# Kernel tuning notes

Hardware: AMD Instinct MI355X
Metric: run time of the kernel (lower is better)

## Reference

```python
import jax, jax.numpy as jnp
import numpy as np

B, T, D = 2, 2048, 2048
H, HD = 8, 128
C = H * HD  # 1024 channels
BT = 64     # chunk size
EPS_RMS = 1.1920929e-07  # torch fp32 finfo eps (RMSNorm default)


def causal_dw_conv(x, w, b):
    # x: [B,T,C], w: [C,4], b: [C]. Equals torch Conv1d(groups=C, k=4, padding=3)[..., :T]
    Bx, Tx, Cx = x.shape
    xp = jnp.pad(x, ((0, 0), (3, 0), (0, 0)))
    out = sum(xp[:, j:j + Tx, :] * w[None, None, :, j] for j in range(4))
    return out + b


def chunk_kda(q, k, v, g):
    # q,k,g: [B,H,T,K]; v: [B,H,T,V]
    Bx, Hx, Tx, K = q.shape
    V = v.shape[-1]
    NT = Tx // BT
    resh = lambda a: a.reshape(Bx, Hx, NT, BT, a.shape[-1])
    q, k, v, g = map(resh, (q, k, v, g))
    gc = jnp.cumsum(g, axis=-2)                        # [B,H,NT,BT,K]
    diff = gc[..., :, None, :] - gc[..., None, :, :]   # [B,H,NT,BT,BT,K]
    tri_incl = jnp.tril(jnp.ones((BT, BT), bool))
    tri_strict = jnp.tril(jnp.ones((BT, BT), bool), -1)
    Aqk = jnp.einsum('bhnik,bhnjk,bhnijk->bhnij', q, k, jnp.exp(diff)) * tri_incl
    Akk = jnp.einsum('bhnik,bhnjk,bhnijk->bhnij', k, k, jnp.exp(-diff)) * tri_strict
    # UT transform: the in-place forward substitution in the source computes
    # A = (I + strictly_lower(Akk))^{-1}; apply it via a unit-lower triangular solve.
    M = Akk + jnp.eye(BT, dtype=q.dtype)
    rhs = jnp.concatenate([jnp.exp(gc) * k, v], axis=-1)
    sol = jax.scipy.linalg.solve_triangular(M, rhs, lower=True, unit_diagonal=True)
    w_, u = sol[..., :K], sol[..., K:]                 # w = A@(exp(gc)*k), u = A@v
    qg = q * jnp.exp(gc)

    def step(S, xs):
        qg_i, k_i, u_i, gc_i, w_i, Aqk_i = xs
        o_i = qg_i @ S + Aqk_i @ (u_i - w_i @ S)
        g_last = gc_i[:, :, -1]                        # [B,H,K]
        decay = jnp.exp(g_last[:, :, None, :] - gc_i)  # [B,H,BT,K]
        S = S * jnp.exp(g_last)[..., :, None] + jnp.einsum('bhck,bhcv->bhkv', k_i * decay, u_i)
        return S, o_i

    xs = tuple(jnp.moveaxis(a, 2, 0) for a in (qg, k, u, gc, w_, Aqk))
    S0 = jnp.zeros((Bx, Hx, K, V), q.dtype)
    S, o = jax.lax.scan(step, S0, xs)
    o = jnp.moveaxis(o, 0, 2).reshape(Bx, Hx, Tx, V)
    return o, S


def _forward(x, Wq, Wk, Wv, conv_q_w, conv_q_b, conv_k_w, conv_k_b, conv_v_w, conv_v_b,
             Wad, Wau, Wb, Wgd, Wgu, norm_w, Wo):
    Bx, Tx, Dx = x.shape
    heads = lambda y: y.reshape(Bx, Tx, H, HD).transpose(0, 2, 1, 3)
    q = heads(causal_dw_conv(x @ Wq, conv_q_w, conv_q_b))
    k = heads(causal_dw_conv(x @ Wk, conv_k_w, conv_k_b))
    q = q / jnp.maximum(jnp.linalg.norm(q, axis=-1, keepdims=True), 1e-12)
    k = k / jnp.maximum(jnp.linalg.norm(k, axis=-1, keepdims=True), 1e-12)
    v = heads(jax.nn.silu(causal_dw_conv(x @ Wv, conv_v_w, conv_v_b)))
    alpha = jax.nn.sigmoid(heads(x @ Wad @ Wau))
    g = jnp.log(jnp.clip(alpha, 1e-6, None))
    _beta = jax.nn.sigmoid(x @ Wb)  # computed in source but unused by chunk_kda
    o, S = chunk_kda(q, k, v, g)
    o = o.transpose(0, 2, 1, 3)                        # [B,T,H,HD]
    o = o * jax.lax.rsqrt(jnp.mean(o * o, axis=-1, keepdims=True) + EPS_RMS) * norm_w
    gate = jax.nn.sigmoid(x @ Wgd @ Wgu).reshape(Bx, Tx, H, HD)
    o = (o * gate).reshape(Bx, Tx, H * HD)
    return o @ Wo, S


def setup_inputs():
    key = jax.random.key(0)
    ks = jax.random.split(key, 16)
    n = lambda k, shape, s=0.02: jax.random.normal(k, shape, jnp.float32) * s
    return {
        'x': jax.random.normal(ks[0], (B, T, D), jnp.float32),
        'Wq': n(ks[1], (D, C)), 'Wk': n(ks[2], (D, C)), 'Wv': n(ks[3], (D, C)),
        'conv_q_w': n(ks[4], (C, 4), 0.1), 'conv_q_b': jnp.zeros((C,), jnp.float32),
        'conv_k_w': n(ks[5], (C, 4), 0.1), 'conv_k_b': jnp.zeros((C,), jnp.float32),
        'conv_v_w': n(ks[6], (C, 4), 0.1), 'conv_v_b': jnp.zeros((C,), jnp.float32),
        'Wad': n(ks[7], (D, HD)), 'Wau': n(ks[8], (HD, C)),
        'Wb': n(ks[9], (D, H)),
        'Wgd': n(ks[10], (D, HD)), 'Wgu': n(ks[11], (HD, C)),
        'norm_w': jnp.ones((HD,), jnp.float32),
        'Wo': n(ks[12], (C, D)),
    }


def reference(x, Wq, Wk, Wv, conv_q_w, conv_q_b, conv_k_w, conv_k_b, conv_v_w, conv_v_b,
              Wad, Wau, Wb, Wgd, Wgu, norm_w, Wo):
    return _forward(x, Wq, Wk, Wv, conv_q_w, conv_q_b, conv_k_w, conv_k_b, conv_v_w, conv_v_b,
                    Wad, Wau, Wb, Wgd, Wgu, norm_w, Wo)
```

## Files before the change

### kernel.cpp

```cpp
#include <hip/hip_runtime.h>
#include <hip/hip_bf16.h>
#include <cstdint>
#include <cstddef>

constexpr int B_  = 2;
constexpr int T_  = 2048;
constexpr int D_  = 2048;
constexpr int H_  = 8;
constexpr int HD_ = 128;
constexpr int C_  = 1024;
constexpr int BT_ = 64;
constexpr int NT_ = 32;
constexpr int M_  = 4096;
constexpr float EPS_RMS = 1.1920929e-07f;

typedef __bf16 bf16x8 __attribute__((ext_vector_type(8)));
typedef float f32x4 __attribute__((ext_vector_type(4)));

typedef const __attribute__((address_space(1))) unsigned int* gptr_t;
typedef __attribute__((address_space(3))) unsigned int* lptr_t;

__device__ __forceinline__ void gload16(const void* g, void* l) {
  __builtin_amdgcn_global_load_lds((gptr_t)g, (lptr_t)l, 16, 0, 0);
}


#define LD_A(base, mq, dst) do { \
    _Pragma("unroll") for (int i_ = 0; i_ < 4; ++i_) \
      _Pragma("unroll") for (int k_ = 0; k_ < 2; ++k_) \
        dst[i_][k_] = *(const bf16x8*)((base) + (mq) * 8192 + i_ * 2048 + k_ * 1024); \
  } while (0)

#define LD_B(base, nq, dst) do { \
    _Pragma("unroll") for (int j_ = 0; j_ < 2; ++j_) \
      _Pragma("unroll") for (int k_ = 0; k_ < 2; ++k_) \
        dst[j_][k_] = *(const bf16x8*)((base) + (nq) * 4096 + j_ * 2048 + k_ * 1024); \
  } while (0)

#define MM_Q(afr, bfr, mq, nq) do { \
    _Pragma("unroll") for (int i_ = 0; i_ < 4; ++i_) \
      _Pragma("unroll") for (int j_ = 0; j_ < 2; ++j_) \
        _Pragma("unroll") for (int k_ = 0; k_ < 2; ++k_) \
          acc[(mq) * 4 + i_][(nq) * 2 + j_] = __builtin_amdgcn_mfma_f32_16x16x32_bf16( \
              afr[i_][k_], bfr[j_][k_], acc[(mq) * 4 + i_][(nq) * 2 + j_], 0, 0, 0); \
  } while (0)

#define STAGE(src, grow0, kc, loff) do { \
    gload16((src) + (size_t)((grow0) + sr0) * 2048 + (kc) + sc0, smem + (loff) + tid * 16); \
    gload16((src) + (size_t)((grow0) + sr1) * 2048 + (kc) + sc1, smem + (loff) + 8192 + tid * 16); \
  } while (0)

#define PH_SYNC_PRE do { \
    __builtin_amdgcn_s_barrier(); \
    asm volatile("s_waitcnt lgkmcnt(0)" ::: "memory"); \
    __builtin_amdgcn_sched_barrier(0); \
    __builtin_amdgcn_s_setprio(1); \
  } while (0)

#define PH_SYNC_POST do { \
    __builtin_amdgcn_s_setprio(0); \
    __builtin_amdgcn_sched_barrier(0); \
    __builtin_amdgcn_s_barrier(); \
  } while (0)

#define PH_SYNC_POST_VM4 do { \
    __builtin_amdgcn_s_setprio(0); \
    __builtin_amdgcn_sched_barrier(0); \
    asm volatile("s_waitcnt vmcnt(4)" ::: "memory"); \
    __builtin_amdgcn_s_barrier(); \
  } while (0)

#define PH_SYNC_POST_VM0 do { \
    __builtin_amdgcn_s_setprio(0); \
    __builtin_amdgcn_sched_barrier(0); \
    asm volatile("s_waitcnt vmcnt(0)" ::: "memory"); \
    __builtin_amdgcn_s_barrier(); \
  } while (0)

__global__ __launch_bounds__(512, 1) void gemm8p(
    const __hip_bfloat16* __restrict__ A_, const __hip_bfloat16* __restrict__ B_,
    __hip_bfloat16* __restrict__ pre, __hip_bfloat16* __restrict__ adb,
    __hip_bfloat16* __restrict__ gdb) {
  __shared__ alignas(16) char smem[131072];
  const int tid = threadIdx.x, lane = tid & 63;
  const int wid = tid >> 6;
  const int wm = (wid >> 2) * 128, wn = (wid & 3) * 64;
  const int lr = lane & 15, lg = lane >> 4;

  const int bid = blockIdx.x;
  const int swz = (bid & 7) * 26 + (bid >> 3);
  const int mt = swz / 13, nt = swz % 13;
  const int m0 = mt * 256, n0g = nt * 256;

  int ob0 = tid * 16;         ob0 ^= ((ob0 >> 9) & 1) << 5;
  int ob1 = (tid + 512) * 16; ob1 ^= ((ob1 >> 9) & 1) << 5;
  const int sr0 = ((ob0 >> 11) << 4) + ((ob0 >> 6) & 15);
  const int sc0 = ((ob0 >> 10) & 1) * 32 + ((ob0 & 63) >> 1);
  const int sr1 = ((ob1 >> 11) << 4) + ((ob1 >> 6) & 15);
  const int sc1 = ((ob1 >> 10) & 1) * 32 + ((ob1 & 63) >> 1);

  const int foff = lr * 64 + ((lg * 16) ^ ((lr & 8) << 2));
  const int bq = (wn & 64) * 128;
  const char* a0base = smem + (wm >> 7) * 16384 + foff;
  const char* a1base = smem + 65536 + (wm >> 7) * 16384 + foff;
  const char* b0base = smem + 32768 + (wn >> 7) * 16384 + bq + foff;
  const char* b1base = smem + 98304 + (wn >> 7) * 16384 + bq + foff;

  f32x4 acc[8][4];
#pragma unroll
  for (int i = 0; i < 8; ++i)
#pragma unroll
    for (int j = 0; j < 4; ++j) acc[i][j] = (f32x4)(0.f);

  bf16x8 a[4][2], b01[2][2], b23[2][2];

  STAGE(A_, m0,        0, 0);
  STAGE(A_, m0 + 128,  0, 16384);
  STAGE(B_, n0g,       0, 32768);
  STAGE(B_, n0g + 128, 0, 32768 + 16384);
  STAGE(B_, n0g,       64, 98304);
  STAGE(B_, n0g + 128, 64, 98304 + 16384);
  asm volatile("s_waitcnt vmcnt(4)" ::: "memory");
  __builtin_amdgcn_s_barrier();

#pragma unroll 1
  for (int it = 0; it < 15; ++it) {
    const int kA1 = (2 * it + 1) * 64;
    const int kN2 = (2 * it + 2) * 64;
    const int kB3 = (2 * it + 3) * 64;
    LD_A(a0base, 0, a);
    LD_B(b0base, 0, b01);
    STAGE(A_, m0, kA1, 65536);
    PH_SYNC_PRE; MM_Q(a, b01, 0, 0); PH_SYNC_POST;
    LD_B(b0base, 1, b23);
    STAGE(A_, m0 + 128, kA1, 65536 + 16384);
    PH_SYNC_PRE; MM_Q(a, b23, 0, 1); PH_SYNC_POST;
    LD_A(a0base, 1, a);
    STAGE(B_, n0g, kN2, 32768);
    PH_SYNC_PRE; MM_Q(a, b23, 1, 1); PH_SYNC_POST;
    STAGE(B_, n0g + 128, kN2, 32768 + 16384);
    PH_SYNC_PRE; MM_Q(a, b01, 1, 0); PH_SYNC_POST_VM4;
    LD_A(a1base, 0, a);
    LD_B(b1base, 0, b01);
    STAGE(A_, m0, kN2, 0);
    PH_SYNC_PRE; MM_Q(a, b01, 0, 0); PH_SYNC_POST;
    LD_B(b1base, 1, b23);
    STAGE(A_, m0 + 128, kN2, 16384);
    PH_SYNC_PRE; MM_Q(a, b23, 0, 1); PH_SYNC_POST;
    LD_A(a1base, 1, a);
    STAGE(B_, n0g, kB3, 98304);
    PH_SYNC_PRE; MM_Q(a, b23, 1, 1); PH_SYNC_POST;
    STAGE(B_, n0g + 128, kB3, 98304 + 16384);
    PH_SYNC_PRE; MM_Q(a, b01, 1, 0); PH_SYNC_POST_VM4;
  }

  {
    const int kT = 1984;
    LD_A(a0base, 0, a);
    LD_B(b0base, 0, b01);
    STAGE(A_, m0, kT, 65536);
    PH_SYNC_PRE; MM_Q(a, b01, 0, 0); PH_SYNC_POST;
    LD_B(b0base, 1, b23);
    STAGE(A_, m0 + 128, kT, 65536 + 16384);
    PH_SYNC_PRE; MM_Q(a, b23, 0, 1); PH_SYNC_POST;
    LD_A(a0base, 1, a);
    PH_SYNC_PRE; MM_Q(a, b23, 1, 1); PH_SYNC_POST;
    PH_SYNC_PRE; MM_Q(a, b01, 1, 0); PH_SYNC_POST_VM0;
    LD_A(a1base, 0, a);
    LD_B(b1base, 0, b01);
    MM_Q(a, b01, 0, 0);
    LD_B(b1base, 1, b23);
    MM_Q(a, b23, 0, 1);
    LD_A(a1base, 1, a);
    MM_Q(a, b23, 1, 1);
    MM_Q(a, b01, 1, 0);
  }

#pragma unroll
  for (int mf = 0; mf < 8; ++mf) {
    const int row0 = m0 + wm + mf * 16 + lg * 4;
#pragma unroll
    for (int nf = 0; nf < 4; ++nf) {
      const int c = n0g + wn + nf * 16 + lr;
#pragma unroll
      for (int r = 0; r < 4; ++r) {
        const __hip_bfloat16 v = __float2bfloat16(acc[mf][nf][r]);
        const size_t rr = (size_t)(row0 + r);
        if (c < 3072)      pre[rr * 3072 + c] = v;
        else if (c < 3200) adb[rr * 128 + (c - 3072)] = v;
        else               gdb[rr * 128 + (c - 3200)] = v;
      }
    }
  }
}

template <typename OutT>
__global__ __launch_bounds__(256) void gemm_bf16k(
    const __hip_bfloat16* __restrict__ A, const __hip_bfloat16* __restrict__ Bt,
    OutT* __restrict__ C, int N, int K) {
  __shared__ __hip_bfloat16 sA[128 * 32];
  __shared__ __hip_bfloat16 sB[128 * 32];
  const int tid = threadIdx.x;
  const int lane = tid & 63;
  const int m0 = blockIdx.y * 128, n0 = blockIdx.x * 128;
  const int wm = ((tid >> 6) >> 1) * 64, wn = ((tid >> 6) & 1) * 64;
  f32x4 acc[4][4];
#pragma unroll
  for (int i = 0; i < 4; ++i)
#pragma unroll
    for (int j = 0; j < 4; ++j) acc[i][j] = (f32x4)(0.f);
  const int f0 = tid, f1 = tid + 256;
  const int r0 = f0 >> 2, c0 = (f0 & 3) * 8;
  const int r1 = f1 >> 2, c1 = (f1 & 3) * 8;
  const size_t aoff0 = (size_t)(m0 + r0) * K + c0;
  const size_t aoff1 = (size_t)(m0 + r1) * K + c1;
  const size_t boff0 = (size_t)(n0 + r0) * K + c0;
  const size_t boff1 = (size_t)(n0 + r1) * K + c1;
  const int lr = lane & 15, lk = (lane >> 4) * 8;
  for (int k0 = 0; k0 < K; k0 += 32) {
    __syncthreads();
    gload16(A + aoff0 + k0, &sA[f0 * 8]);
    gload16(A + aoff1 + k0, &sA[f1 * 8]);
    gload16(Bt + boff0 + k0, &sB[f0 * 8]);
    gload16(Bt + boff1 + k0, &sB[f1 * 8]);
    __syncthreads();
    bf16x8 af[4], bfr[4];
#pragma unroll
    for (int i = 0; i < 4; ++i)
      af[i] = *(const bf16x8*)&sA[(wm + i * 16 + lr) * 32 + lk];
#pragma unroll
    for (int j = 0; j < 4; ++j)
      bfr[j] = *(const bf16x8*)&sB[(wn + j * 16 + lr) * 32 + lk];
#pragma unroll
    for (int i = 0; i < 4; ++i)
#pragma unroll
      for (int j = 0; j < 4; ++j)
        acc[i][j] = __builtin_amdgcn_mfma_f32_16x16x32_bf16(af[i], bfr[j], acc[i][j], 0, 0, 0);
  }
  const int er = (lane >> 4) * 4, ec = lane & 15;
#pragma unroll
  for (int i = 0; i < 4; ++i) {
#pragma unroll
    for (int j = 0; j < 4; ++j) {
      int row = m0 + wm + i * 16 + er;
      int col = n0 + wn + j * 16 + ec;
#pragma unroll
      for (int r = 0; r < 4; ++r) {
        float v = acc[i][j][r];
        if constexpr (sizeof(OutT) == 2)
          C[(size_t)(row + r) * N + col] = __float2bfloat16(v);
        else
          C[(size_t)(row + r) * N + col] = v;
      }
    }
  }
}

__global__ __launch_bounds__(256) void gemm_augu(
    const __hip_bfloat16* __restrict__ ad, const __hip_bfloat16* __restrict__ gd,
    const __hip_bfloat16* __restrict__ Wau, const __hip_bfloat16* __restrict__ Wgu,
    float* __restrict__ gc, float* __restrict__ glast,
    __hip_bfloat16* __restrict__ gatef) {
  constexpr int N = 1024, K = 128;
  __shared__ alignas(16) char smraw[128 * 132 * 4];
  __hip_bfloat16* sA = (__hip_bfloat16*)smraw;
  __hip_bfloat16* sB = (__hip_bfloat16*)(smraw + 8192);
  float (*scan)[132] = (float(*)[132])smraw;

  const int z = blockIdx.z;
  const __hip_bfloat16* A = z ? gd : ad;
  const __hip_bfloat16* Bt = z ? Wgu : Wau;
  const int tid = threadIdx.x;
  const int lane = tid & 63;
  const int m0 = blockIdx.y * 128, n0 = blockIdx.x * 128;
  const int wm = ((tid >> 6) >> 1) * 64, wn = ((tid >> 6) & 1) * 64;
  f32x4 acc[4][4];
#pragma unroll
  for (int i = 0; i < 4; ++i)
#pragma unroll
    for (int j = 0; j < 4; ++j) acc[i][j] = (f32x4)(0.f);
  const int f0 = tid, f1 = tid + 256;
  const int r0 = f0 >> 2, c0 = (f0 & 3) * 8;
  const int r1 = f1 >> 2, c1 = (f1 & 3) * 8;
  const size_t aoff0 = (size_t)(m0 + r0) * K + c0;
  const size_t aoff1 = (size_t)(m0 + r1) * K + c1;
  const size_t boff0 = (size_t)(n0 + r0) * K + c0;
  const size_t boff1 = (size_t)(n0 + r1) * K + c1;
  const int lr = lane & 15, lk = (lane >> 4) * 8;
#pragma unroll
  for (int k0 = 0; k0 < K; k0 += 32) {
    __syncthreads();
    gload16(A + aoff0 + k0, &sA[f0 * 8]);
    gload16(A + aoff1 + k0, &sA[f1 * 8]);
    gload16(Bt + boff0 + k0, &sB[f0 * 8]);
    gload16(Bt + boff1 + k0, &sB[f1 * 8]);
    __syncthreads();
    bf16x8 af[4], bfr[4];
#pragma unroll
    for (int i = 0; i < 4; ++i)
      af[i] = *(const bf16x8*)&sA[(wm + i * 16 + lr) * 32 + lk];
#pragma unroll
    for (int j = 0; j < 4; ++j)
      bfr[j] = *(const bf16x8*)&sB[(wn + j * 16 + lr) * 32 + lk];
#pragma unroll
    for (int i = 0; i < 4; ++i)
#pragma unroll
      for (int j = 0; j < 4; ++j)
        acc[i][j] = __builtin_amdgcn_mfma_f32_16x16x32_bf16(af[i], bfr[j], acc[i][j], 0, 0, 0);
  }
  const int er = (lane >> 4) * 4, ec = lane & 15;
  if (z == 1) {
#pragma unroll
    for (int i = 0; i < 4; ++i)
#pragma unroll
      for (int j = 0; j < 4; ++j) {
        int row = m0 + wm + i * 16 + er;
        int col = n0 + wn + j * 16 + ec;
#pragma unroll
        for (int r = 0; r < 4; ++r)
          gatef[(size_t)(row + r) * N + col] = __float2bfloat16(acc[i][j][r]);
      }
    return;
  }
  __syncthreads();
#pragma unroll
  for (int i = 0; i < 4; ++i)
#pragma unroll
    for (int j = 0; j < 4; ++j) {
      int rowL = wm + i * 16 + er;
      int colL = wn + j * 16 + ec;
#pragma unroll
      for (int r = 0; r < 4; ++r) {
        float a = acc[i][j][r];
        float s = fmaxf(1.f / (1.f + __expf(-a)), 1e-6f);
        scan[rowL + r][colL] = __logf(s);
      }
    }
  __syncthreads();
  {
    const int d = tid & 127, c2 = tid >> 7;
    const int h = blockIdx.x;
    const int b = m0 >> 11, tb = m0 & 2047;
    const int bh = b * H_ + h;
    float run = 0.f;
    const size_t gbase = ((size_t)bh * T_ + tb + c2 * 64) * 128 + d;
    for (int r = 0; r < 64; ++r) {
      run += scan[c2 * 64 + r][d];
      gc[gbase + (size_t)r * 128] = run;
    }
    glast[((size_t)(bh * NT_ + (tb >> 6) + c2)) * 128 + d] = run;
  }
}

__global__ __launch_bounds__(256) void prep(
    const float* __restrict__ x, const float* __restrict__ Wq,
    const float* __restrict__ Wk, const float* __restrict__ Wv,
    const float* __restrict__ Wad, const float* __restrict__ Wgd,
    const float* __restrict__ Wau, const float* __restrict__ Wgu,
    const float* __restrict__ Wo, __hip_bfloat16* __restrict__ xb,
    __hip_bfloat16* __restrict__ Wt_qkv, __hip_bfloat16* __restrict__ Wt_dg,
    __hip_bfloat16* __restrict__ Wt_aug, __hip_bfloat16* __restrict__ Wt_o) {
  __shared__ float tile[32][33];
  int bid = blockIdx.x;
  const int tid = threadIdx.x;
  if (bid < 8192) {
    size_t i = ((size_t)bid * 256 + tid) * 4;
    float4 v = *(const float4*)(x + i);
    union { __hip_bfloat16 hx[4]; uint2 u2; } pk_;
    pk_.hx[0] = __float2bfloat16(v.x);
    pk_.hx[1] = __float2bfloat16(v.y);
    pk_.hx[2] = __float2bfloat16(v.z);
    pk_.hx[3] = __float2bfloat16(v.w);
    *(uint2*)(xb + i) = pk_.u2;
    return;
  }
  bid -= 8192;
  const float* W; __hip_bfloat16* dst; int K, N, bx, by;
  if (bid < 6144) {
    int z = bid / 2048, r = bid % 2048;
    W = (z == 0) ? Wq : (z == 1) ? Wk : Wv;
    dst = Wt_qkv + (size_t)z * C_ * D_;
    K = D_; N = C_; bx = r & 31; by = r >> 5;
  } else if (bid < 6144 + 512) {
    int b2 = bid - 6144;
    int z = b2 >> 8, r = b2 & 255;
    W = z ? Wgd : Wad;
    dst = Wt_dg + (size_t)z * HD_ * D_;
    K = D_; N = HD_; bx = r & 3; by = r >> 2;
  } else if (bid < 6144 + 512 + 256) {
    int b2 = bid - 6144 - 512;
    int z = b2 >> 7, r = b2 & 127;
    W = z ? Wgu : Wau;
    dst = Wt_aug + (size_t)z * C_ * HD_;
    K = HD_; N = C_; bx = r & 31; by = r >> 5;
  } else {
    int b2 = bid - 6144 - 512 - 256;
    W = Wo; dst = Wt_o;
    K = C_; N = D_; bx = b2 & 63; by = b2 >> 6;
  }
  int tx = tid & 31, ty = tid >> 5;
  int kb = by * 32, nb = bx * 32;
#pragma unroll
  for (int s = 0; s < 4; ++s) {
    int kk = ty + s * 8;
    tile[kk][tx] = W[(size_t)(kb + kk) * N + nb + tx];
  }
  __syncthreads();
#pragma unroll
  for (int s = 0; s < 4; ++s) {
    int nn = ty + s * 8;
    dst[(size_t)(nb + nn) * K + kb + tx] = __float2bfloat16(tile[tx][nn]);
  }
}

__global__ __launch_bounds__(256) void conv_qkv(
    const __hip_bfloat16* __restrict__ pre, const float* __restrict__ gc,
    const float* __restrict__ cqw, const float* __restrict__ cqb,
    const float* __restrict__ ckw, const float* __restrict__ ckb,
    const float* __restrict__ cvw, const float* __restrict__ cvb,
    __hip_bfloat16* __restrict__ qg, __hip_bfloat16* __restrict__ kp,
    __hip_bfloat16* __restrict__ km, __hip_bfloat16* __restrict__ vb) {
  const int bhn = blockIdx.x;
  const int b = bhn >> 8, h = (bhn >> 5) & 7, n = bhn & 31;
  const int wv = threadIdx.x >> 6, lane = threadIdx.x & 63;
  const int d0 = lane * 2;
  const int c0 = h * HD_ + d0;

  float qw[2][4], kw[2][4], vw[2][4], qb2[2], kb2[2], vb2[2];
#pragma unroll
  for (int e = 0; e < 2; ++e) {
    const int c = c0 + e;
#pragma unroll
    for (int j = 0; j < 4; ++j) {
      qw[e][j] = cqw[c * 4 + j];
      kw[e][j] = ckw[c * 4 + j];
      vw[e][j] = cvw[c * 4 + j];
    }
    qb2[e] = cqb[c]; kb2[e] = ckb[c]; vb2[e] = cvb[c];
  }

  const int tw0 = n * 64 + wv * 16;
  const size_t prow0 = ((size_t)b * T_ + tw0) * (3 * C_) + c0;

  float xm[3][3][2];
#pragma unroll
  for (int a = 0; a < 3; ++a)
#pragma unroll
    for (int g2 = 0; g2 < 3; ++g2) { xm[a][g2][0] = 0.f; xm[a][g2][1] = 0.f; }
#pragma unroll
  for (int g2 = 1; g2 <= 3; ++g2) {
    if (tw0 - g2 >= 0) {
      const __hip_bfloat16* pr = pre + (prow0 - (size_t)g2 * (3 * C_));
#pragma unroll
      for (int a = 0; a < 3; ++a) {
        uint u = *(const uint*)(pr + a * C_);
        xm[a][g2 - 1][0] = __bfloat162float(((const __hip_bfloat16*)&u)[0]);
        xm[a][g2 - 1][1] = __bfloat162float(((const __hip_bfloat16*)&u)[1]);
      }
    }
  }

#pragma unroll
  for (int i = 0; i < 16; ++i) {
    const int t = tw0 + i;
    const __hip_bfloat16* pr = pre + (prow0 + (size_t)i * (3 * C_));
    float x0[3][2];
#pragma unroll
    for (int a = 0; a < 3; ++a) {
      uint u = *(const uint*)(pr + a * C_);
      x0[a][0] = __bfloat162float(((const __hip_bfloat16*)&u)[0]);
      x0[a][1] = __bfloat162float(((const __hip_bfloat16*)&u)[1]);
    }
    float aq[2], ak[2], av[2];
#pragma unroll
    for (int e = 0; e < 2; ++e) {
      aq[e] = qb2[e] + qw[e][3] * x0[0][e];
      if (t > 0) aq[e] += qw[e][2] * xm[0][0][e];
      if (t > 1) aq[e] += qw[e][1] * xm[0][1][e];
      if (t > 2) aq[e] += qw[e][0] * xm[0][2][e];
      ak[e] = kb2[e] + kw[e][3] * x0[1][e];
      if (t > 0) ak[e] += kw[e][2] * xm[1][0][e];
      if (t > 1) ak[e] += kw[e][1] * xm[1][1][e];
      if (t > 2) ak[e] += kw[e][0] * xm[1][2][e];
      av[e] = vb2[e] + vw[e][3] * x0[2][e];
      if (t > 0) av[e] += vw[e][2] * xm[2][0][e];
      if (t > 1) av[e] += vw[e][1] * xm[2][1][e];
      if (t > 2) av[e] += vw[e][0] * xm[2][2][e];
    }
#pragma unroll
    for (int a = 0; a < 3; ++a) {
#pragma unroll
      for (int e = 0; e < 2; ++e) {
        xm[a][2][e] = xm[a][1][e];
        xm[a][1][e] = xm[a][0][e];
        xm[a][0][e] = x0[a][e];
      }
    }
    float ssq = aq[0] * aq[0] + aq[1] * aq[1];
    float ssk = ak[0] * ak[0] + ak[1] * ak[1];
#pragma unroll
    for (int o = 1; o < 64; o <<= 1) {
      ssq += __shfl_xor(ssq, o);
      ssk += __shfl_xor(ssk, o);
    }
    const float nq = fmaxf(sqrtf(ssq), 1e-12f);
    const float nk = fmaxf(sqrtf(ssk), 1e-12f);
    const size_t oi = (((size_t)b * H_ + h) * T_ + t) * HD_ + d0;
    const float2 gv = *(const float2*)(gc + oi);
    union { __hip_bfloat16 hx[2]; uint u; } oq, okp, okm, ov;
#pragma unroll
    for (int e = 0; e < 2; ++e) {
      const float g = (e == 0) ? gv.x : gv.y;
      const float eg = __expf(g), emg = __expf(-g);
      oq.hx[e]  = __float2bfloat16(aq[e] / nq * eg);
      const float kn = ak[e] / nk;
      okp.hx[e] = __float2bfloat16(kn * eg);
      okm.hx[e] = __float2bfloat16(kn * emg);
      ov.hx[e]  = __float2bfloat16(av[e] * (1.f / (1.f + __expf(-av[e]))));
    }
    *(uint*)(qg + oi) = oq.u;
    *(uint*)(kp + oi) = okp.u;
    *(uint*)(km + oi) = okm.u;
    *(uint*)(vb + oi) = ov.u;
  }
}

__global__ __launch_bounds__(512) void chunk_mid(
    const __hip_bfloat16* __restrict__ qg, const __hip_bfloat16* __restrict__ kp,
    const __hip_bfloat16* __restrict__ km, const __hip_bfloat16* __restrict__ vb,
    __hip_bfloat16* __restrict__ Aq, __hip_bfloat16* __restrict__ w_bf,
    __hip_bfloat16* __restrict__ u_bf, __hip_bfloat16* __restrict__ PT_bf) {
  __shared__ float A_T[64][68];
  __shared__ float solu[64][128];
  __shared__ __hip_bfloat16 kmS[64 * 128];
  const int tid = threadIdx.x;
  const int bhn = blockIdx.x;
  const size_t gbase = ((size_t)(bhn >> 5) * T_ + (size_t)(bhn & 31) * BT_) * HD_;
  const int wv = tid >> 6, lane = tid & 63;
  const int lr = lane & 15, lg = lane >> 4;
  const int prod = wv >> 2, rh = wv & 3;

  {
    const char* src = (const char*)(km + gbase);
#pragma unroll
    for (int s = 0; s < 2; ++s)
      gload16(src + s * 8192 + tid * 16, ((char*)kmS) + s * 8192 + tid * 16);
  }

  {
    const __hip_bfloat16* A = (prod ? qg : km) + gbase;
    const __hip_bfloat16* Bt = (prod ? km : kp) + gbase;
    f32x4 acc[4];
#pragma unroll
    for (int j = 0; j < 4; ++j) acc[j] = (f32x4)(0.f);
#pragma unroll
    for (int k0 = 0; k0 < 128; k0 += 32) {
      bf16x8 af, bfr[4];
      af = *(const bf16x8*)(A + (size_t)(rh * 16 + lr) * 128 + k0 + lg * 8);
#pragma unroll
      for (int j = 0; j < 4; ++j)
        bfr[j] = *(const bf16x8*)(Bt + (size_t)(j * 16 + lr) * 128 + k0 + lg * 8);
#pragma unroll
      for (int j = 0; j < 4; ++j)
        acc[j] = __builtin_amdgcn_mfma_f32_16x16x32_bf16(af, bfr[j], acc[j], 0, 0, 0);
    }
    if (prod == 0) {
#pragma unroll
      for (int j = 0; j < 4; ++j) {
        int row0 = rh * 16 + lg * 4;
        int col = j * 16 + lr;
        *(float4*)&A_T[col][row0] =
            make_float4(acc[j][0], acc[j][1], acc[j][2], acc[j][3]);
      }
    } else {
      __hip_bfloat16* dst = Aq + (size_t)bhn * 4096;
#pragma unroll
      for (int j = 0; j < 4; ++j)
#pragma unroll
        for (int r = 0; r < 4; ++r) {
          int row = rh * 16 + lg * 4 + r;
          int col = j * 16 + lr;
          float v = (col <= row) ? acc[j][r] : 0.f;
          dst[row * 64 + col] = __float2bfloat16(v);
        }
    }
  }
  __syncthreads();

  if (tid < 256) {
    const int col = tid & 127;
    const __hip_bfloat16* rhs = ((tid < 128) ? kp : vb) + gbase;
    float s[64];
#pragma unroll
    for (int i = 0; i < 64; ++i)
      s[i] = __bfloat162float(rhs[(size_t)i * 128 + col]);
#pragma unroll
    for (int ib = 0; ib < 64; ib += 4) {
      const float s0 = s[ib];
      const float s1 = fmaf(-A_T[ib][ib + 1], s0, s[ib + 1]);
      const float s2 = fmaf(-A_T[ib + 1][ib + 2], s1,
                       fmaf(-A_T[ib][ib + 2], s0, s[ib + 2]));
      const float s3 = fmaf(-A_T[ib + 2][ib + 3], s2,
                       fmaf(-A_T[ib + 1][ib + 3], s1,
                       fmaf(-A_T[ib][ib + 3], s0, s[ib + 3])));
      s[ib + 1] = s1; s[ib + 2] = s2; s[ib + 3] = s3;
#pragma unroll
      for (int j4 = ib + 4; j4 < 64; j4 += 4) {
        float4 a0 = *(const float4*)&A_T[ib][j4];
        float4 a1 = *(const float4*)&A_T[ib + 1][j4];
        float4 a2 = *(const float4*)&A_T[ib + 2][j4];
        float4 a3 = *(const float4*)&A_T[ib + 3][j4];
        s[j4]     = fmaf(-a3.x, s3, fmaf(-a2.x, s2, fmaf(-a1.x, s1, fmaf(-a0.x, s0, s[j4]))));
        s[j4 + 1] = fmaf(-a3.y, s3, fmaf(-a2.y, s2, fmaf(-a1.y, s1, fmaf(-a0.y, s0, s[j4 + 1]))));
        s[j4 + 2] = fmaf(-a3.z, s3, fmaf(-a2.z, s2, fmaf(-a1.z, s1, fmaf(-a0.z, s0, s[j4 + 2]))));
        s[j4 + 3] = fmaf(-a3.w, s3, fmaf(-a2.w, s2, fmaf(-a1.w, s1, fmaf(-a0.w, s0, s[j4 + 3]))));
      }
    }
    if (tid < 128) {
#pragma unroll
      for (int i = 0; i < 64; ++i)
        w_bf[gbase + (size_t)i * 128 + col] = __float2bfloat16(s[i]);
    } else {
#pragma unroll
      for (int i = 0; i < 64; ++i) {
        u_bf[gbase + (size_t)i * 128 + col] = __float2bfloat16(s[i]);
        solu[i][col] = s[i];
      }
    }
  }
  __syncthreads();

  {
    const int kd0 = (tid & 15) * 8, vd0 = (tid >> 4) * 4;
    float acc[8][4];
#pragma unroll
    for (int a = 0; a < 8; ++a)
#pragma unroll
      for (int b2 = 0; b2 < 4; ++b2) acc[a][b2] = 0.f;
#pragma unroll 4
    for (int i = 0; i < 64; ++i) {
      uint4 rawv = *(const uint4*)&kmS[i * 128 + kd0];
      const __hip_bfloat16* hp = (const __hip_bfloat16*)&rawv;
      float kv[8];
#pragma unroll
      for (int e = 0; e < 8; ++e) kv[e] = __bfloat162float(hp[e]);
      float4 uv = *(const float4*)&solu[i][vd0];
#pragma unroll
      for (int a = 0; a < 8; ++a) {
        acc[a][0] = fmaf(kv[a], uv.x, acc[a][0]);
        acc[a][1] = fmaf(kv[a], uv.y, acc[a][1]);
        acc[a][2] = fmaf(kv[a], uv.z, acc[a][2]);
        acc[a][3] = fmaf(kv[a], uv.w, acc[a][3]);
      }
    }
    __hip_bfloat16* dst = PT_bf + (size_t)bhn * 16384;
#pragma unroll
    for (int b2 = 0; b2 < 4; ++b2) {
      union { __hip_bfloat16 hx[8]; uint4 u4; } pk2;
#pragma unroll
      for (int a = 0; a < 8; ++a) pk2.hx[a] = __float2bfloat16(acc[a][b2]);
      *(uint4*)(dst + (size_t)(vd0 + b2) * 128 + kd0) = pk2.u4;
    }
  }
}

__global__ __launch_bounds__(128) void scan_pt(
    const __hip_bfloat16* __restrict__ PT_bf, const float* __restrict__ glast,
    __hip_bfloat16* __restrict__ STg, float* __restrict__ Sout) {
  int vd = blockIdx.x & 127;
  int bh = blockIdx.x >> 7;
  int kd = threadIdx.x;
  float s = 0.f;
  for (int n = 0; n < NT_; ++n) {
    size_t idx = (((size_t)bh * NT_ + n) * HD_ + vd) * HD_ + kd;
    float p = __bfloat162float(PT_bf[idx]);
    STg[idx] = __float2bfloat16(s);
    float gl = glast[((size_t)bh * NT_ + n) * 128 + kd];
    s = (s + p) * __expf(gl);
  }
  Sout[((size_t)bh * HD_ + kd) * HD_ + vd] = s;
}

__global__ __launch_bounds__(512) void chunk_tail(
    const __hip_bfloat16* __restrict__ qg_bf, const __hip_bfloat16* __restrict__ w_bf,
    const __hip_bfloat16* __restrict__ u_bf, const __hip_bfloat16* __restrict__ Aq_bf,
    const __hip_bfloat16* __restrict__ STg, const __hip_bfloat16* __restrict__ gatef,
    const float* __restrict__ normw, __hip_bfloat16* __restrict__ o2b) {
  constexpr int XTS = 72;
  __shared__ __hip_bfloat16 XT[128 * XTS];
  __shared__ float red[64][4];
  __shared__ __hip_bfloat16 uS[64 * 128];
  const int tid = threadIdx.x;
  const int bhn = blockIdx.x;
  const int bh = bhn >> 5, n = bhn & 31;
  const int b = bh >> 3, h = bh & 7;
  const int t0 = n * 64, hoff = h * 128;
  const size_t gbase = ((size_t)bh * T_ + t0) * 128;
  const __hip_bfloat16* Sg = STg + (size_t)bhn * 16384;

  {
    const char* src = (const char*)(u_bf + gbase);
#pragma unroll
    for (int s = 0; s < 2; ++s)
      gload16(src + s * 8192 + tid * 16, ((char*)uS) + s * 8192 + tid * 16);
  }

  const int wv = tid >> 6, lane = tid & 63;
  const int lr = lane & 15, lg = lane >> 4;
  const int rowh = wv >> 2, colq = wv & 3;
  f32x4 accX[2][2], accO[2][2];
#pragma unroll
  for (int i = 0; i < 2; ++i)
#pragma unroll
    for (int j = 0; j < 2; ++j) { accX[i][j] = (f32x4)(0.f); accO[i][j] = (f32x4)(0.f); }

  const __hip_bfloat16* wrow = w_bf + gbase;
  const __hip_bfloat16* qrow = qg_bf + gbase;
#pragma unroll
  for (int k0 = 0; k0 < 128; k0 += 32) {
    bf16x8 aW[2], aQ[2], bS[2];
#pragma unroll
    for (int i = 0; i < 2; ++i) {
      aW[i] = *(const bf16x8*)(wrow + (size_t)(rowh * 32 + i * 16 + lr) * 128 + k0 + lg * 8);
      aQ[i] = *(const bf16x8*)(qrow + (size_t)(rowh * 32 + i * 16 + lr) * 128 + k0 + lg * 8);
    }
#pragma unroll
    for (int j = 0; j < 2; ++j)
      bS[j] = *(const bf16x8*)(Sg + (size_t)(colq * 32 + j * 16 + lr) * 128 + k0 + lg * 8);
#pragma unroll
    for (int i = 0; i < 2; ++i)
#pragma unroll
      for (int j = 0; j < 2; ++j) {
        accX[i][j] = __builtin_amdgcn_mfma_f32_16x16x32_bf16(aW[i], bS[j], accX[i][j], 0, 0, 0);
        accO[i][j] = __builtin_amdgcn_mfma_f32_16x16x32_bf16(aQ[i], bS[j], accO[i][j], 0, 0, 0);
      }
  }

  asm volatile("s_waitcnt vmcnt(0)" ::: "memory");
  __builtin_amdgcn_s_barrier();

#pragma unroll
  for (int i = 0; i < 2; ++i)
#pragma unroll
    for (int j = 0; j < 2; ++j) {
      int row0 = rowh * 32 + i * 16 + lg * 4;
      int col = colq * 32 + j * 16 + lr;
      union { __hip_bfloat16 hx[4]; uint2 u2; } xv;
#pragma unroll
      for (int r = 0; r < 4; ++r) {
        float uu = __bfloat162float(uS[(row0 + r) * 128 + col]);
        xv.hx[r] = __float2bfloat16(uu - accX[i][j][r]);
      }
      *(uint2*)&XT[col * XTS + row0] = xv.u2;
    }
  __syncthreads();

  const __hip_bfloat16* aqb = Aq_bf + (size_t)bhn * 4096;
#pragma unroll
  for (int k0 = 0; k0 < 64; k0 += 32) {
    bf16x8 aA[2], bX[2];
#pragma unroll
    for (int i = 0; i < 2; ++i)
      aA[i] = *(const bf16x8*)(aqb + (size_t)(rowh * 32 + i * 16 + lr) * 64 + k0 + lg * 8);
#pragma unroll
    for (int j = 0; j < 2; ++j)
      bX[j] = *(const bf16x8*)&XT[(colq * 32 + j * 16 + lr) * XTS + k0 + lg * 8];
#pragma unroll
    for (int i = 0; i < 2; ++i)
#pragma unroll
      for (int j = 0; j < 2; ++j)
        accO[i][j] = __builtin_amdgcn_mfma_f32_16x16x32_bf16(aA[i], bX[j], accO[i][j], 0, 0, 0);
  }

#pragma unroll
  for (int i = 0; i < 2; ++i)
#pragma unroll
    for (int r = 0; r < 4; ++r) {
      int row = rowh * 32 + i * 16 + lg * 4 + r;
      float o0 = accO[i][0][r], o1 = accO[i][1][r];
      float ss = o0 * o0 + o1 * o1;
#pragma unroll
      for (int o = 1; o < 16; o <<= 1) ss += __shfl_xor(ss, o);
      if (lr == 0) red[row][colq] = ss;
    }
  __syncthreads();
  float nw0 = normw[colq * 32 + lr];
  float nw1 = normw[colq * 32 + 16 + lr];
#pragma unroll
  for (int i = 0; i < 2; ++i)
#pragma unroll
    for (int r = 0; r < 4; ++r) {
      int row = rowh * 32 + i * 16 + lg * 4 + r;
      float tot = red[row][0] + red[row][1] + red[row][2] + red[row][3];
      float rms = rsqrtf(tot * (1.f / 128.f) + EPS_RMS);
      size_t orow = (size_t)(b * T_ + t0 + row) * C_ + hoff;
      int c0 = colq * 32 + lr, c1 = c0 + 16;
      float g0 = __bfloat162float(gatef[orow + c0]);
      float g1 = __bfloat162float(gatef[orow + c1]);
      float s0 = 1.f / (1.f + __expf(-g0));
      float s1 = 1.f / (1.f + __expf(-g1));
      o2b[orow + c0] = __float2bfloat16(accO[i][0][r] * rms * nw0 * s0);
      o2b[orow + c1] = __float2bfloat16(accO[i][1][r] * rms * nw1 * s1);
    }
}

extern "C" void kernel_launch(void* const* d_in, const int* in_sizes, int n_in,
                              void* d_out, int out_size, void* d_ws, size_t ws_size,
                              hipStream_t stream) {
  (void)in_sizes; (void)n_in; (void)out_size;
  const float* x    = (const float*)d_in[0];
  const float* Wq   = (const float*)d_in[1];
  const float* Wk   = (const float*)d_in[2];
  const float* Wv   = (const float*)d_in[3];
  const float* cqw  = (const float*)d_in[4];
  const float* cqb  = (const float*)d_in[5];
  const float* ckw  = (const float*)d_in[6];
  const float* ckb  = (const float*)d_in[7];
  const float* cvw  = (const float*)d_in[8];
  const float* cvb  = (const float*)d_in[9];
  const float* Wad  = (const float*)d_in[10];
  const float* Wau  = (const float*)d_in[11];
  const float* Wgd  = (const float*)d_in[13];
  const float* Wgu  = (const float*)d_in[14];
  const float* normw= (const float*)d_in[15];
  const float* Wo   = (const float*)d_in[16];

  float* outp = (float*)d_out;
  float* Sout = outp + (size_t)M_ * D_;

  const size_t SZ = (size_t)M_ * C_;

  float* ws = (float*)d_ws;
  __hip_bfloat16* pre_qkv = (__hip_bfloat16*)(ws);
  float* a_full = ws + 3 * SZ / 2;
  __hip_bfloat16* gatef = (__hip_bfloat16*)(ws + 5 * SZ / 2);
  float* gc_g = ws + 3 * SZ;
  __hip_bfloat16* qg_bf = (__hip_bfloat16*)(ws + 4 * SZ);
  __hip_bfloat16* kp_bf = (__hip_bfloat16*)(ws + 9 * SZ / 2);
  __hip_bfloat16* km_bf = (__hip_bfloat16*)(ws + 5 * SZ);
  __hip_bfloat16* v_bf  = (__hip_bfloat16*)(ws + 11 * SZ / 2);
  __hip_bfloat16* w_bf  = (__hip_bfloat16*)(ws + 6 * SZ);
  __hip_bfloat16* u_bf  = (__hip_bfloat16*)(ws + 13 * SZ / 2);
  __hip_bfloat16* Aq_bf = (__hip_bfloat16*)(ws + 7 * SZ);
  float* glast = ws + 29 * SZ / 4;
  __hip_bfloat16* PT_bf = (__hip_bfloat16*)(ws + 15 * SZ / 2);
  __hip_bfloat16* STg   = (__hip_bfloat16*)(ws + 17 * SZ / 2);
  __hip_bfloat16* xb    = (__hip_bfloat16*)(ws + 19 * SZ / 2);
  __hip_bfloat16* Wt_qkv = (__hip_bfloat16*)(ws + 21 * SZ / 2);
  size_t off = 21 * SZ / 2 + 3 * SZ / 4;
  __hip_bfloat16* Wt_dg  = (__hip_bfloat16*)(ws + off); off += 262144;
  __hip_bfloat16* Wt_aug = (__hip_bfloat16*)(ws + off); off += 131072;
  __hip_bfloat16* Wt_o   = (__hip_bfloat16*)(ws + off); off += 1048576;
  __hip_bfloat16* ad_bf  = (__hip_bfloat16*)(ws + off); off += 262144;
  __hip_bfloat16* gd_bf  = (__hip_bfloat16*)(ws + off); off += 262144;
  if (ws_size < off * sizeof(float)) return;

  __hip_bfloat16* o2b = (__hip_bfloat16*)a_full;
  __hip_bfloat16* Wt_au = Wt_aug;
  __hip_bfloat16* Wt_gu = Wt_aug + (size_t)C_ * HD_;

  prep<<<17152, 256, 0, stream>>>(x, Wq, Wk, Wv, Wad, Wgd, Wau, Wgu, Wo,
                                  xb, Wt_qkv, Wt_dg, Wt_aug, Wt_o);

  gemm8p<<<208, 512, 0, stream>>>(xb, Wt_qkv, pre_qkv, ad_bf, gd_bf);
  gemm_augu<<<dim3(C_ / 128, M_ / 128, 2), 256, 0, stream>>>(
      ad_bf, gd_bf, Wt_au, Wt_gu, gc_g, glast, gatef);

  conv_qkv<<<B_ * H_ * NT_, 256, 0, stream>>>(pre_qkv, gc_g, cqw, cqb, ckw, ckb,
                                              cvw, cvb, qg_bf, kp_bf, km_bf, v_bf);

  chunk_mid<<<B_ * H_ * NT_, 512, 0, stream>>>(qg_bf, kp_bf, km_bf, v_bf,
                                               Aq_bf, w_bf, u_bf, PT_bf);
  scan_pt<<<B_ * H_ * HD_, 128, 0, stream>>>(PT_bf, glast, STg, Sout);

  chunk_tail<<<B_ * H_ * NT_, 512, 0, stream>>>(qg_bf, w_bf, u_bf, Aq_bf, STg,
                                                gatef, normw, o2b);
  gemm_bf16k<float><<<dim3(D_ / 128, M_ / 128), 256, 0, stream>>>(o2b, Wt_o, outp, D_, C_);
}
```

Measured before the change: 340.6 us.

## Fuse causal conv/normalization into chunk_mid, keeping k and v in swizzled LDS

Removes the separate conv_qkv kernel and computes the depthwise conv, L2 norm, gating exponentials and SiLU inside chunk_mid, with 8 waves each producing 8 rows of the chunk. The kp, km and v tiles now stay in XOR-swizzled shared memory instead of making a round trip through global memory. Only qg is still written to global, because chunk_tail reads it. This saves a kernel launch and about three global write/read passes. In exchange, shared memory grows to about 65 KB, the solu buffer is aliased onto the kp/v region with an extra barrier, and occupancy may drop.

```diff
diff --git a/kernel.cpp b/kernel.cpp
--- a/kernel.cpp
+++ b/kernel.cpp
@@ -23,6 +23,8 @@
 __device__ __forceinline__ void gload16(const void* g, void* l) {
   __builtin_amdgcn_global_load_lds((gptr_t)g, (lptr_t)l, 16, 0, 0);
 }
+
+#define SWZ(row, cbytes) ((((row) * 256) + (cbytes)) ^ (((row) & 7) << 4))
 
 
 #define LD_A(base, mq, dst) do { \
@@ -413,153 +415,150 @@
   }
 }
 
-__global__ __launch_bounds__(256) void conv_qkv(
+__global__ __launch_bounds__(512) void chunk_mid(
     const __hip_bfloat16* __restrict__ pre, const float* __restrict__ gc,
     const float* __restrict__ cqw, const float* __restrict__ cqb,
     const float* __restrict__ ckw, const float* __restrict__ ckb,
     const float* __restrict__ cvw, const float* __restrict__ cvb,
-    __hip_bfloat16* __restrict__ qg, __hip_bfloat16* __restrict__ kp,
-    __hip_bfloat16* __restrict__ km, __hip_bfloat16* __restrict__ vb) {
+    __hip_bfloat16* __restrict__ qg, __hip_bfloat16* __restrict__ Aq,
+    __hip_bfloat16* __restrict__ w_bf, __hip_bfloat16* __restrict__ u_bf,
+    __hip_bfloat16* __restrict__ PT_bf) {
+  __shared__ alignas(16) char smc[66560];
+  char* kpL = smc;
+  char* vbL = smc + 16384;
+  char* kmL = smc + 32768;
+  float (*A_T)[68] = (float(*)[68])(smc + 49152);
+  float* solu = (float*)smc;
+
+  const int tid = threadIdx.x;
   const int bhn = blockIdx.x;
-  const int b = bhn >> 8, h = (bhn >> 5) & 7, n = bhn & 31;
-  const int wv = threadIdx.x >> 6, lane = threadIdx.x & 63;
-  const int d0 = lane * 2;
-  const int c0 = h * HD_ + d0;
-
-  float qw[2][4], kw[2][4], vw[2][4], qb2[2], kb2[2], vb2[2];
-#pragma unroll
-  for (int e = 0; e < 2; ++e) {
-    const int c = c0 + e;
-#pragma unroll
-    for (int j = 0; j < 4; ++j) {
-      qw[e][j] = cqw[c * 4 + j];
-      kw[e][j] = ckw[c * 4 + j];
-      vw[e][j] = cvw[c * 4 + j];
-    }
-    qb2[e] = cqb[c]; kb2[e] = ckb[c]; vb2[e] = cvb[c];
-  }
-
-  const int tw0 = n * 64 + wv * 16;
-  const size_t prow0 = ((size_t)b * T_ + tw0) * (3 * C_) + c0;
-
-  float xm[3][3][2];
-#pragma unroll
-  for (int a = 0; a < 3; ++a)
-#pragma unroll
-    for (int g2 = 0; g2 < 3; ++g2) { xm[a][g2][0] = 0.f; xm[a][g2][1] = 0.f; }
-#pragma unroll
-  for (int g2 = 1; g2 <= 3; ++g2) {
-    if (tw0 - g2 >= 0) {
-      const __hip_bfloat16* pr = pre + (prow0 - (size_t)g2 * (3 * C_));
+  const int bh = bhn >> 5, n = bhn & 31;
+  const int b = bh >> 3, h = bh & 7;
+  const size_t gbase = ((size_t)bh * T_ + (size_t)n * BT_) * HD_;
+  const int wv = tid >> 6, lane = tid & 63;
+  const int lr = lane & 15, lg = lane >> 4;
+
+  {
+    const int d0 = lane * 2;
+    const int c0 = h * HD_ + d0;
+    float qw[2][4], kw[2][4], vw[2][4], qb2[2], kb2[2], vb2[2];
+#pragma unroll
+    for (int e = 0; e < 2; ++e) {
+      const int c = c0 + e;
+#pragma unroll
+      for (int j = 0; j < 4; ++j) {
+        qw[e][j] = cqw[c * 4 + j];
+        kw[e][j] = ckw[c * 4 + j];
+        vw[e][j] = cvw[c * 4 + j];
+      }
+      qb2[e] = cqb[c]; kb2[e] = ckb[c]; vb2[e] = cvb[c];
+    }
+    const int tw0 = n * 64 + wv * 8;
+    const size_t prow0 = ((size_t)b * T_ + tw0) * (3 * C_) + c0;
+    float xm[3][3][2];
+#pragma unroll
+    for (int a = 0; a < 3; ++a)
+#pragma unroll
+      for (int g2 = 0; g2 < 3; ++g2) { xm[a][g2][0] = 0.f; xm[a][g2][1] = 0.f; }
+#pragma unroll
+    for (int g2 = 1; g2 <= 3; ++g2) {
+      if (tw0 - g2 >= 0) {
+        const __hip_bfloat16* pr = pre + (prow0 - (size_t)g2 * (3 * C_));
+#pragma unroll
+        for (int a = 0; a < 3; ++a) {
+          uint u = *(const uint*)(pr + a * C_);
+          xm[a][g2 - 1][0] = __bfloat162float(((const __hip_bfloat16*)&u)[0]);
+          xm[a][g2 - 1][1] = __bfloat162float(((const __hip_bfloat16*)&u)[1]);
+        }
+      }
+    }
+#pragma unroll
+    for (int i = 0; i < 8; ++i) {
+      const int t = tw0 + i;
+      const __hip_bfloat16* pr = pre + (prow0 + (size_t)i * (3 * C_));
+      float x0[3][2];
 #pragma unroll
       for (int a = 0; a < 3; ++a) {
         uint u = *(const uint*)(pr + a * C_);
-        xm[a][g2 - 1][0] = __bfloat162float(((const __hip_bfloat16*)&u)[0]);
-        xm[a][g2 - 1][1] = __bfloat162float(((const __hip_bfloat16*)&u)[1]);
-      }
-    }
-  }
-
-#pragma unroll
-  for (int i = 0; i < 16; ++i) {
-    const int t = tw0 + i;
-    const __hip_bfloat16* pr = pre + (prow0 + (size_t)i * (3 * C_));
-    float x0[3][2];
-#pragma unroll
-    for (int a = 0; a < 3; ++a) {
-      uint u = *(const uint*)(pr + a * C_);
-      x0[a][0] = __bfloat162float(((const __hip_bfloat16*)&u)[0]);
-      x0[a][1] = __bfloat162float(((const __hip_bfloat16*)&u)[1]);
-    }
-    float aq[2], ak[2], av[2];
-#pragma unroll
-    for (int e = 0; e < 2; ++e) {
-      aq[e] = qb2[e] + qw[e][3] * x0[0][e];
-      if (t > 0) aq[e] += qw[e][2] * xm[0][0][e];
-      if (t > 1) aq[e] += qw[e][1] * xm[0][1][e];
-      if (t > 2) aq[e] += qw[e][0] * xm[0][2][e];
-      ak[e] = kb2[e] + kw[e][3] * x0[1][e];
-      if (t > 0) ak[e] += kw[e][2] * xm[1][0][e];
-      if (t > 1) ak[e] += kw[e][1] * xm[1][1][e];
-      if (t > 2) ak[e] += kw[e][0] * xm[1][2][e];
-      av[e] = vb2[e] + vw[e][3] * x0[2][e];
-      if (t > 0) av[e] += vw[e][2] * xm[2][0][e];
-      if (t > 1) av[e] += vw[e][1] * xm[2][1][e];
-      if (t > 2) av[e] += vw[e][0] * xm[2][2][e];
-    }
-#pragma unroll
-    for (int a = 0; a < 3; ++a) {
+        x0[a][0] = __bfloat162float(((const __hip_bfloat16*)&u)[0]);
+        x0[a][1] = __bfloat162float(((const __hip_bfloat16*)&u)[1]);
+      }
+      float aq[2], ak[2], av[2];
 #pragma unroll
       for (int e = 0; e < 2; ++e) {
-        xm[a][2][e] = xm[a][1][e];
-        xm[a][1][e] = xm[a][0][e];
-        xm[a][0][e] = x0[a][e];
-      }
-    }
-    float ssq = aq[0] * aq[0] + aq[1] * aq[1];
-    float ssk = ak[0] * ak[0] + ak[1] * ak[1];
-#pragma unroll
-    for (int o = 1; o < 64; o <<= 1) {
-      ssq += __shfl_xor(ssq, o);
-      ssk += __shfl_xor(ssk, o);
-    }
-    const float nq = fmaxf(sqrtf(ssq), 1e-12f);
-    const float nk = fmaxf(sqrtf(ssk), 1e-12f);
-    const size_t oi = (((size_t)b * H_ + h) * T_ + t) * HD_ + d0;
-    const float2 gv = *(const float2*)(gc + oi);
-    union { __hip_bfloat16 hx[2]; uint u; } oq, okp, okm, ov;
-#pragma unroll
-    for (int e = 0; e < 2; ++e) {
-      const float g = (e == 0) ? gv.x : gv.y;
-      const float eg = __expf(g), emg = __expf(-g);
-      oq.hx[e]  = __float2bfloat16(aq[e] / nq * eg);
-      const float kn = ak[e] / nk;
-      okp.hx[e] = __float2bfloat16(kn * eg);
-      okm.hx[e] = __float2bfloat16(kn * emg);
-      ov.hx[e]  = __float2bfloat16(av[e] * (1.f / (1.f + __expf(-av[e]))));
-    }
-    *(uint*)(qg + oi) = oq.u;
-    *(uint*)(kp + oi) = okp.u;
-    *(uint*)(km + oi) = okm.u;
-    *(uint*)(vb + oi) = ov.u;
-  }
-}
-
-__global__ __launch_bounds__(512) void chunk_mid(
-    const __hip_bfloat16* __restrict__ qg, const __hip_bfloat16* __restrict__ kp,
-    const __hip_bfloat16* __restrict__ km, const __hip_bfloat16* __restrict__ vb,
-    __hip_bfloat16* __restrict__ Aq, __hip_bfloat16* __restrict__ w_bf,
-    __hip_bfloat16* __restrict__ u_bf, __hip_bfloat16* __restrict__ PT_bf) {
-  __shared__ float A_T[64][68];
-  __shared__ float solu[64][128];
-  __shared__ __hip_bfloat16 kmS[64 * 128];
-  const int tid = threadIdx.x;
-  const int bhn = blockIdx.x;
-  const size_t gbase = ((size_t)(bhn >> 5) * T_ + (size_t)(bhn & 31) * BT_) * HD_;
-  const int wv = tid >> 6, lane = tid & 63;
-  const int lr = lane & 15, lg = lane >> 4;
-  const int prod = wv >> 2, rh = wv & 3;
+        aq[e] = qb2[e] + qw[e][3] * x0[0][e];
+        if (t > 0) aq[e] += qw[e][2] * xm[0][0][e];
+        if (t > 1) aq[e] += qw[e][1] * xm[0][1][e];
+        if (t > 2) aq[e] += qw[e][0] * xm[0][2][e];
+        ak[e] = kb2[e] + kw[e][3] * x0[1][e];
+        if (t > 0) ak[e] += kw[e][2] * xm[1][0][e];
+        if (t > 1) ak[e] += kw[e][1] * xm[1][1][e];
+        if (t > 2) ak[e] += kw[e][0] * xm[1][2][e];
+        av[e] = vb2[e] + vw[e][3] * x0[2][e];
+        if (t > 0) av[e] += vw[e][2] * xm[2][0][e];
+        if (t > 1) av[e] += vw[e][1] * xm[2][1][e];
+        if (t > 2) av[e] += vw[e][0] * xm[2][2][e];
+      }
+#pragma unroll
+      for (int a = 0; a < 3; ++a) {
+#pragma unroll
+        for (int e = 0; e < 2; ++e) {
+          xm[a][2][e] = xm[a][1][e];
+          xm[a][1][e] = xm[a][0][e];
+          xm[a][0][e] = x0[a][e];
+        }
+      }
+      float ssq = aq[0] * aq[0] + aq[1] * aq[1];
+      float ssk = ak[0] * ak[0] + ak[1] * ak[1];
+#pragma unroll
+      for (int o = 1; o < 64; o <<= 1) {
+        ssq += __shfl_xor(ssq, o);
+        ssk += __shfl_xor(ssk, o);
+      }
+      const float nq = fmaxf(sqrtf(ssq), 1e-12f);
+      const float nk = fmaxf(sqrtf(ssk), 1e-12f);
+      const int row = wv * 8 + i;
+      const size_t oi = gbase + (size_t)row * 128 + d0;
+      const float2 gv = *(const float2*)(gc + oi);
+      union { __hip_bfloat16 hx[2]; uint u; } oq, okp, okm, ov;
+#pragma unroll
+      for (int e = 0; e < 2; ++e) {
+        const float g = (e == 0) ? gv.x : gv.y;
+        const float eg = __expf(g), emg = __expf(-g);
+        oq.hx[e]  = __float2bfloat16(aq[e] / nq * eg);
+        const float kn = ak[e] / nk;
+        okp.hx[e] = __float2bfloat16(kn * eg);
+        okm.hx[e] = __float2bfloat16(kn * emg);
+        ov.hx[e]  = __float2bfloat16(av[e] * (1.f / (1.f + __expf(-av[e]))));
+      }
+      *(uint*)(qg + oi) = oq.u;
+      *(uint*)(kpL + SWZ(row, d0 * 2)) = okp.u;
+      *(uint*)(kmL + SWZ(row, d0 * 2)) = okm.u;
+      *(uint*)(vbL + SWZ(row, d0 * 2)) = ov.u;
+    }
+  }
+  __syncthreads();
 
   {
-    const char* src = (const char*)(km + gbase);
-#pragma unroll
-    for (int s = 0; s < 2; ++s)
-      gload16(src + s * 8192 + tid * 16, ((char*)kmS) + s * 8192 + tid * 16);
-  }
-
-  {
-    const __hip_bfloat16* A = (prod ? qg : km) + gbase;
-    const __hip_bfloat16* Bt = (prod ? km : kp) + gbase;
+    const int prod = wv >> 2, rh = wv & 3;
     f32x4 acc[4];
 #pragma unroll
     for (int j = 0; j < 4; ++j) acc[j] = (f32x4)(0.f);
 #pragma unroll
     for (int k0 = 0; k0 < 128; k0 += 32) {
       bf16x8 af, bfr[4];
-      af = *(const bf16x8*)(A + (size_t)(rh * 16 + lr) * 128 + k0 + lg * 8);
-#pragma unroll
-      for (int j = 0; j < 4; ++j)
-        bfr[j] = *(const bf16x8*)(Bt + (size_t)(j * 16 + lr) * 128 + k0 + lg * 8);
+      const int ar = rh * 16 + lr;
+      if (prod == 0)
+        af = *(const bf16x8*)(kmL + SWZ(ar, (k0 + lg * 8) * 2));
+      else
+        af = *(const bf16x8*)(qg + gbase + (size_t)ar * 128 + k0 + lg * 8);
+#pragma unroll
+      for (int j = 0; j < 4; ++j) {
+        const int br = j * 16 + lr;
+        bfr[j] = (prod == 0)
+          ? *(const bf16x8*)(kpL + SWZ(br, (k0 + lg * 8) * 2))
+          : *(const bf16x8*)(kmL + SWZ(br, (k0 + lg * 8) * 2));
+      }
 #pragma unroll
       for (int j = 0; j < 4; ++j)
         acc[j] = __builtin_amdgcn_mfma_f32_16x16x32_bf16(af, bfr[j], acc[j], 0, 0, 0);
@@ -587,13 +586,17 @@
   }
   __syncthreads();
 
+  float s[64];
+  const int col = tid & 127;
   if (tid < 256) {
-    const int col = tid & 127;
-    const __hip_bfloat16* rhs = ((tid < 128) ? kp : vb) + gbase;
-    float s[64];
+    const char* rhsL = (tid < 128) ? kpL : vbL;
 #pragma unroll
     for (int i = 0; i < 64; ++i)
-      s[i] = __bfloat162float(rhs[(size_t)i * 128 + col]);
+      s[i] = __bfloat162float(*(const __hip_bfloat16*)(rhsL + SWZ(i, col * 2)));
+  }
+  __syncthreads();
+
+  if (tid < 256) {
 #pragma unroll
     for (int ib = 0; ib < 64; ib += 4) {
       const float s0 = s[ib];
@@ -624,7 +627,7 @@
 #pragma unroll
       for (int i = 0; i < 64; ++i) {
         u_bf[gbase + (size_t)i * 128 + col] = __float2bfloat16(s[i]);
-        solu[i][col] = s[i];
+        solu[i * 128 + col] = s[i];
       }
     }
   }
@@ -639,12 +642,12 @@
       for (int b2 = 0; b2 < 4; ++b2) acc[a][b2] = 0.f;
 #pragma unroll 4
     for (int i = 0; i < 64; ++i) {
-      uint4 rawv = *(const uint4*)&kmS[i * 128 + kd0];
+      uint4 rawv = *(const uint4*)(kmL + SWZ(i, kd0 * 2));
       const __hip_bfloat16* hp = (const __hip_bfloat16*)&rawv;
       float kv[8];
 #pragma unroll
       for (int e = 0; e < 8; ++e) kv[e] = __bfloat162float(hp[e]);
-      float4 uv = *(const float4*)&solu[i][vd0];
+      float4 uv = *(const float4*)&solu[i * 128 + vd0];
 #pragma unroll
       for (int a = 0; a < 8; ++a) {
         acc[a][0] = fmaf(kv[a], uv.x, acc[a][0]);
@@ -836,9 +839,6 @@
   __hip_bfloat16* gatef = (__hip_bfloat16*)(ws + 5 * SZ / 2);
   float* gc_g = ws + 3 * SZ;
   __hip_bfloat16* qg_bf = (__hip_bfloat16*)(ws + 4 * SZ);
-  __hip_bfloat16* kp_bf = (__hip_bfloat16*)(ws + 9 * SZ / 2);
-  __hip_bfloat16* km_bf = (__hip_bfloat16*)(ws + 5 * SZ);
-  __hip_bfloat16* v_bf  = (__hip_bfloat16*)(ws + 11 * SZ / 2);
   __hip_bfloat16* w_bf  = (__hip_bfloat16*)(ws + 6 * SZ);
   __hip_bfloat16* u_bf  = (__hip_bfloat16*)(ws + 13 * SZ / 2);
   __hip_bfloat16* Aq_bf = (__hip_bfloat16*)(ws + 7 * SZ);
@@ -866,11 +866,9 @@
   gemm_augu<<<dim3(C_ / 128, M_ / 128, 2), 256, 0, stream>>>(
       ad_bf, gd_bf, Wt_au, Wt_gu, gc_g, glast, gatef);
 
-  conv_qkv<<<B_ * H_ * NT_, 256, 0, stream>>>(pre_qkv, gc_g, cqw, cqb, ckw, ckb,
-                                              cvw, cvb, qg_bf, kp_bf, km_bf, v_bf);
-
-  chunk_mid<<<B_ * H_ * NT_, 512, 0, stream>>>(qg_bf, kp_bf, km_bf, v_bf,
-                                               Aq_bf, w_bf, u_bf, PT_bf);
+  chunk_mid<<<B_ * H_ * NT_, 512, 0, stream>>>(pre_qkv, gc_g, cqw, cqb, ckw, ckb,
+                                               cvw, cvb, qg_bf, Aq_bf, w_bf,
+                                               u_bf, PT_bf);
   scan_pt<<<B_ * H_ * HD_, 128, 0, stream>>>(PT_bf, glast, STg, Sout);
 
   chunk_tail<<<B_ * H_ * NT_, 512, 0, stream>>>(qg_bf, w_bf, u_bf, Aq_bf, STg,
```

After: 336.7 us. Within noise of the previous version (-1.2%).
